# Performance work log

Hardware: AMD Instinct MI355X
Metric: run time of the kernel (lower is better)

Reference implementation:

```python
import jax, jax.numpy as jnp
import numpy as np

B, SQ, SK = 2, 2048, 2048
D, H = 1024, 16
HD = D // H              # head_dim = 64
R = 128                  # rel_pos_max_distance
P = 2 * R + 1            # num_pos_ids = 257
RADIUS = 256             # local_attention_radius


def setup_inputs() -> dict:
    key = jax.random.key(0)
    ks = jax.random.split(key, 8)
    s = 0.02
    return {
        "Q": jax.random.normal(ks[0], (B, SQ, D), dtype=jnp.float32),
        "K": jax.random.normal(ks[1], (B, SK, D), dtype=jnp.float32),
        "V": jax.random.normal(ks[2], (B, SK, D), dtype=jnp.float32),
        "Wq": jax.random.normal(ks[3], (D, D), dtype=jnp.float32) * s,
        "Wk": jax.random.normal(ks[4], (D, D), dtype=jnp.float32) * s,
        "Wv": jax.random.normal(ks[5], (D, D), dtype=jnp.float32) * s,
        "Wo": jax.random.normal(ks[6], (D, D), dtype=jnp.float32) * s,
        "E": jax.random.normal(ks[7], (P, D), dtype=jnp.float32) * s,  # rel_embeds
    }


def _split_heads(x, W):
    # bias-free projection then split: B x S x D -> B x H x S x HD
    y = x @ W.T
    b, s, _ = y.shape
    return y.reshape(b, s, H, HD).transpose(0, 2, 1, 3)


def reference(Q, K, V, Wq, Wk, Wv, Wo, E):
    q = _split_heads(Q, Wq)  # B,H,Sq,HD
    k = _split_heads(K, Wk)  # B,H,Sk,HD
    v = _split_heads(V, Wv)  # B,H,Sk,HD

    # rel_embeds reshape matches torch: E[p] viewed as (head_dim, num_heads)
    rel = E.reshape(P, HD, H).transpose(2, 0, 1)           # H,P,HD
    Q_rel = jnp.einsum("bhqd,hpd->bhqp", q, rel)           # B,H,Sq,P

    # slided relative position ids: clip(j - i, -R, R) + R
    i = jnp.arange(SQ)[:, None]
    j = jnp.arange(SK)[None, :]
    rel_ids = jnp.clip(j - i, -R, R) + R                   # Sq,Sk
    rel_shift = jnp.take_along_axis(
        Q_rel, jnp.broadcast_to(rel_ids, (B, H, SQ, SK)), axis=3
    )                                                       # B,H,Sq,Sk

    energy = (jnp.einsum("bhqd,bhkd->bhqk", q, k) + rel_shift) / jnp.sqrt(
        jnp.float32(HD)
    )

    # local attention mask: True = masked (outside window of radius RADIUS)
    mask = jnp.abs(j - i) > RADIUS                          # Sq,Sk
    mask = mask & ~jnp.all(mask, axis=-1, keepdims=True)    # never mask full rows
    energy = jnp.where(mask[None, None], -jnp.inf, energy)

    attn = jax.nn.softmax(energy, axis=-1)                  # B,H,Sq,Sk
    out = jnp.einsum("bhqk,bhkd->bhqd", attn, v)            # B,H,Sq,HD
    # torch: view(B,H,Sq,HD).permute(0,2,3,1).flatten(2,3) -> B,Sq,(HD*H)
    out = out.transpose(0, 2, 3, 1).reshape(B, SQ, D)
    return out @ Wo.T
```

## Files before the change

### kernel.cpp

```cpp
#include <hip/hip_runtime.h>
#include <hip/hip_bf16.h>

#define BATCH 2
#define SQn 2048
#define SKn 2048
#define DMODEL 1024
#define NH 16
#define HD 64
#define NPOS 257
#define RWIN 128
#define RADIUS 256

typedef __attribute__((ext_vector_type(8))) short bf16x8;
typedef __attribute__((ext_vector_type(4))) float f32x4;

static __device__ __forceinline__ unsigned short f2bf(float f) {
    union { float f; unsigned u; } v; v.f = f;
    unsigned r = (v.u + 0x7FFFu + ((v.u >> 16) & 1u)) >> 16;
    return (unsigned short)r;
}
static __device__ __forceinline__ float bf2f(unsigned short b) {
    union { unsigned u; float f; } v; v.u = ((unsigned)b) << 16;
    return v.f;
}

static __device__ __forceinline__ void gl_lds16(const unsigned short* g, unsigned short* l) {
    __builtin_amdgcn_global_load_lds(
        (const __attribute__((address_space(1))) unsigned*)g,
        (__attribute__((address_space(3))) unsigned*)l, 16, 0, 0);
}

#define SWZ(row) (((row) ^ ((row) >> 2)) & 3)

__global__ __launch_bounds__(256) void convert_kernel(
    const float* __restrict__ Q, const float* __restrict__ K, const float* __restrict__ V,
    const float* __restrict__ Wq, const float* __restrict__ Wk, const float* __restrict__ Wv,
    const float* __restrict__ Wo,
    unsigned short* __restrict__ xb,
    unsigned short* __restrict__ wb,
    unsigned short* __restrict__ wob)
{
    int i = blockIdx.x * 256 + threadIdx.x;
    const float* src;
    unsigned short* dst;
    int off;
    if (i < 3145728) {
        int which = i >> 20;
        off = i & 1048575;
        src = which == 0 ? Q : (which == 1 ? K : V);
        dst = xb + (size_t)which * 4194304;
    } else {
        int i2 = i - 3145728;
        int which = i2 >> 18;
        off = i2 & 262143;
        src = which == 0 ? Wq : (which == 1 ? Wk : (which == 2 ? Wv : Wo));
        dst = which < 3 ? wb + (size_t)which * 1048576 : wob;
    }
    float4 v4 = ((const float4*)src)[off];
    ushort4 o4;
    o4.x = f2bf(v4.x); o4.y = f2bf(v4.y); o4.z = f2bf(v4.z); o4.w = f2bf(v4.w);
    ((ushort4*)dst)[off] = o4;
}

__global__ __launch_bounds__(256) void mfma_gemm(
    const unsigned short* __restrict__ Xall,
    const unsigned short* __restrict__ Wall,
    unsigned short* __restrict__ Yall)
{
    __shared__ unsigned short sA[128 * 32];
    __shared__ unsigned short sB[128 * 32];
    __shared__ unsigned short sT[64 * 136];

    const int tid  = threadIdx.x;
    const int wv   = tid >> 6;
    const int lane = tid & 63;
    const int quad = lane >> 4;
    const int l15  = lane & 15;
    const int z    = blockIdx.z;
    const int m0   = blockIdx.x * 128;
    const int n0   = blockIdx.y * 128;
    const int wr   = (wv >> 1) * 64;
    const int wc   = (wv & 1) * 64;

    const unsigned short* X = Xall + (size_t)z * (4096 * 1024);
    const unsigned short* W = Wall + (size_t)z * (1024 * 1024);

    int aoff[4], boff[4];
#pragma unroll
    for (int t = 0; t < 4; ++t) {
        int row = wr + t * 16 + l15;
        aoff[t] = row * 32 + ((quad ^ SWZ(row)) * 8);
        int col = wc + t * 16 + l15;
        boff[t] = col * 32 + ((quad ^ SWZ(col)) * 8);
    }

    int srow[2], scg[2], sf[2];
#pragma unroll
    for (int r = 0; r < 2; ++r) {
        int f = r * 256 + tid;
        sf[r] = f;
        srow[r] = f >> 2;
        scg[r] = (f & 3) ^ SWZ(srow[r]);
    }

    f32x4 acc[4][4];
#pragma unroll
    for (int i = 0; i < 4; ++i)
#pragma unroll
        for (int j = 0; j < 4; ++j)
            acc[i][j] = (f32x4){0.f, 0.f, 0.f, 0.f};

    for (int k0 = 0; k0 < 1024; k0 += 32) {
        __syncthreads();
#pragma unroll
        for (int r = 0; r < 2; ++r) {
            gl_lds16(X + (size_t)(m0 + srow[r]) * 1024 + k0 + scg[r] * 8, &sA[sf[r] * 8]);
            gl_lds16(W + (size_t)(n0 + srow[r]) * 1024 + k0 + scg[r] * 8, &sB[sf[r] * 8]);
        }
        __syncthreads();

        bf16x8 af[4], bfr[4];
#pragma unroll
        for (int t = 0; t < 4; ++t) af[t]  = *(const bf16x8*)&sA[aoff[t]];
#pragma unroll
        for (int t = 0; t < 4; ++t) bfr[t] = *(const bf16x8*)&sB[boff[t]];
#pragma unroll
        for (int i = 0; i < 4; ++i)
#pragma unroll
            for (int j = 0; j < 4; ++j)
                acc[i][j] = __builtin_amdgcn_mfma_f32_16x16x32_bf16(af[i], bfr[j], acc[i][j], 0, 0, 0);
    }

    unsigned short* Y = Yall + (size_t)z * (4096 * 1024);
    const int b_ = m0 >> 11;
    const int s0 = m0 & (SQn - 1);

    if (z < 2) {
#pragma unroll
        for (int i = 0; i < 4; ++i) {
            int mbase = s0 + wr + i * 16 + quad * 4;
#pragma unroll
            for (int j = 0; j < 4; ++j) {
                int col = n0 + wc + j * 16 + l15;
                int h = col >> 6, dd = col & 63;
                unsigned short* yb = Y + (((size_t)(b_ * NH + h) * SQn) << 6) + dd;
#pragma unroll
                for (int r = 0; r < 4; ++r)
                    yb[(size_t)(mbase + r) << 6] = f2bf(acc[i][j][r]);
            }
        }
    } else {
#pragma unroll
        for (int hh = 0; hh < 2; ++hh) {
            __syncthreads();
            if ((wv & 1) == hh) {
#pragma unroll
                for (int i = 0; i < 4; ++i) {
                    int mloc = wr + i * 16 + quad * 4;
#pragma unroll
                    for (int j = 0; j < 4; ++j) {
                        ushort4 pk;
                        pk.x = f2bf(acc[i][j][0]);
                        pk.y = f2bf(acc[i][j][1]);
                        pk.z = f2bf(acc[i][j][2]);
                        pk.w = f2bf(acc[i][j][3]);
                        *(ushort4*)&sT[(j * 16 + l15) * 136 + mloc] = pk;
                    }
                }
            }
            __syncthreads();
            int h = (n0 >> 6) + hh;
            unsigned short* yb = Y + ((size_t)(b_ * NH + h) * HD) * SKn + s0;
#pragma unroll
            for (int it = 0; it < 4; ++it) {
                int u = it * 256 + tid;
                int dd = u >> 4, mc = u & 15;
                uint4 val = *(const uint4*)&sT[dd * 136 + mc * 8];
                *(uint4*)(yb + (size_t)dd * SKn + mc * 8) = val;
            }
        }
    }
}

__global__ __launch_bounds__(256) void gemm_out(
    const unsigned short* __restrict__ X,
    const unsigned short* __restrict__ W,
    float* __restrict__ Y)
{
    __shared__ unsigned short sA[64 * 32];
    __shared__ unsigned short sB[128 * 32];

    const int tid  = threadIdx.x;
    const int wv   = tid >> 6;
    const int lane = tid & 63;
    const int quad = lane >> 4;
    const int l15  = lane & 15;
    const int m0   = blockIdx.x * 64;
    const int n0   = blockIdx.y * 128;
    const int wr   = (wv >> 1) * 32;
    const int wc   = (wv & 1) * 64;

    int aoff[2], boff[4];
#pragma unroll
    for (int i = 0; i < 2; ++i) {
        int row = wr + i * 16 + l15;
        aoff[i] = row * 32 + ((quad ^ SWZ(row)) * 8);
    }
#pragma unroll
    for (int j = 0; j < 4; ++j) {
        int col = wc + j * 16 + l15;
        boff[j] = col * 32 + ((quad ^ SWZ(col)) * 8);
    }

    const int af_  = tid;
    const int arow = af_ >> 2;
    const int acs  = (af_ & 3) ^ SWZ(arow);
    int bf_[2], brow[2], bcs[2];
#pragma unroll
    for (int r = 0; r < 2; ++r) {
        int f = r * 256 + tid;
        bf_[r] = f; brow[r] = f >> 2; bcs[r] = (f & 3) ^ SWZ(brow[r]);
    }

    f32x4 acc[2][4];
#pragma unroll
    for (int i = 0; i < 2; ++i)
#pragma unroll
        for (int j = 0; j < 4; ++j)
            acc[i][j] = (f32x4){0.f, 0.f, 0.f, 0.f};

    for (int k0 = 0; k0 < 1024; k0 += 32) {
        __syncthreads();
        gl_lds16(X + (size_t)(m0 + arow) * 1024 + k0 + acs * 8, &sA[af_ * 8]);
#pragma unroll
        for (int r = 0; r < 2; ++r)
            gl_lds16(W + (size_t)(n0 + brow[r]) * 1024 + k0 + bcs[r] * 8, &sB[bf_[r] * 8]);
        __syncthreads();

        bf16x8 af[2], bfr[4];
#pragma unroll
        for (int i = 0; i < 2; ++i) af[i]  = *(const bf16x8*)&sA[aoff[i]];
#pragma unroll
        for (int j = 0; j < 4; ++j) bfr[j] = *(const bf16x8*)&sB[boff[j]];
#pragma unroll
        for (int i = 0; i < 2; ++i)
#pragma unroll
            for (int j = 0; j < 4; ++j)
                acc[i][j] = __builtin_amdgcn_mfma_f32_16x16x32_bf16(af[i], bfr[j], acc[i][j], 0, 0, 0);
    }

#pragma unroll
    for (int i = 0; i < 2; ++i) {
        int mbase = m0 + wr + i * 16 + quad * 4;
#pragma unroll
        for (int j = 0; j < 4; ++j) {
            int col = n0 + wc + j * 16 + l15;
#pragma unroll
            for (int r = 0; r < 4; ++r)
                Y[(size_t)(mbase + r) * DMODEL + col] = acc[i][j][r];
        }
    }
}

__global__ __launch_bounds__(256) void relt_kernel(
    const float* __restrict__ E, unsigned short* __restrict__ relTb)
{
    int idx = blockIdx.x * 256 + threadIdx.x;
    const int total = NH * NPOS * HD;
    if (idx < total) {
        int d = idx & (HD - 1);
        int p = (idx >> 6) % NPOS;
        int h = idx / (NPOS * HD);
        relTb[idx] = f2bf(E[(size_t)p * DMODEL + d * NH + h]);
    }
}

#define BIAS_S 9.765625e-4f

__global__ __launch_bounds__(256) void attn_mfma(
    const unsigned short* __restrict__ q,
    const unsigned short* __restrict__ k,
    const unsigned short* __restrict__ vT,
    const unsigned short* __restrict__ relTb,
    unsigned short* __restrict__ aob)
{
    __shared__ unsigned short sQ[64 * 64];
    __shared__ unsigned short sK[64 * 64];
    __shared__ unsigned short sVt[64 * 64];
    __shared__ unsigned short sP[4][16 * 72];
    __shared__ signed char    sq8[64 * 260];

    const int tid  = threadIdx.x;
    const int w    = tid >> 6;
    const int lane = tid & 63;
    const int quad = lane >> 4;
    const int l15  = lane & 15;
    const int xcd  = blockIdx.x & 7;
    const int sidx = blockIdx.x >> 3;
    const int bh   = (xcd << 2) | (sidx >> 5);
    const int q0   = (sidx & 31) << 6;
    const int h    = bh & (NH - 1);
    const int b    = bh >> 4;

    const int f1 = tid,       row1 = f1 >> 3;
    const int c1 = ((f1 & 7) ^ (row1 & 7)) * 8;
    const int f2 = 256 + tid, row2 = f2 >> 3;
    const int c2 = ((f2 & 7) ^ (row2 & 7)) * 8;

    {
        const unsigned short* gq = q + ((size_t)bh * SQn + q0) * HD;
        gl_lds16(gq + row1 * HD + c1, &sQ[f1 * 8]);
        gl_lds16(gq + row2 * HD + c2, &sQ[f2 * 8]);
    }
    __syncthreads();

    const int qrow = w * 16 + l15;
    const int qs = (quad ^ (qrow & 7)) * 8;
    bf16x8 a0 = *(const bf16x8*)&sQ[qrow * 64 + qs];
    bf16x8 a1 = *(const bf16x8*)&sQ[qrow * 64 + (qs ^ 32)];

    const int myrow = w * 16 + quad * 4;
    for (int c5 = 0; c5 < 5; ++c5) {
        __syncthreads();
        const unsigned short* gr = relTb + ((size_t)h * NPOS + c5 * 64) * HD;
        gl_lds16(gr + row1 * HD + c1, &sK[f1 * 8]);
        gl_lds16(gr + row2 * HD + c2, &sK[f2 * 8]);
        __syncthreads();
#pragma unroll
        for (int t = 0; t < 4; ++t) {
            int prow = t * 16 + l15;
            int ks = (quad ^ (prow & 7)) * 8;
            bf16x8 b0 = *(const bf16x8*)&sK[prow * 64 + ks];
            bf16x8 b1 = *(const bf16x8*)&sK[prow * 64 + (ks ^ 32)];
            f32x4 cc = {0.f, 0.f, 0.f, 0.f};
            cc = __builtin_amdgcn_mfma_f32_16x16x32_bf16(a0, b0, cc, 0, 0, 0);
            cc = __builtin_amdgcn_mfma_f32_16x16x32_bf16(a1, b1, cc, 0, 0, 0);
            int pos = c5 * 64 + t * 16 + l15;
            if (pos < NPOS) {
#pragma unroll
                for (int r = 0; r < 4; ++r) {
                    int iq = (int)rintf(cc[r] * 128.0f);
                    iq = iq < -127 ? -127 : (iq > 127 ? 127 : iq);
                    sq8[(myrow + r) * 260 + pos] = (signed char)iq;
                }
            }
        }
    }
    __syncthreads();

    float bias0[4], bias256[4];
#pragma unroll
    for (int r = 0; r < 4; ++r) {
        bias0[r]   = (float)sq8[(myrow + r) * 260 + 0]   * BIAS_S;
        bias256[r] = (float)sq8[(myrow + r) * 260 + 256] * BIAS_S;
    }

    const int lo = (q0 - RADIUS) > 0 ? (q0 - RADIUS) : 0;
    const int hi = (q0 + 63 + RADIUS) < (SKn - 1) ? (q0 + 63 + RADIUS) : (SKn - 1);
    const int nt = ((hi - lo) >> 6) + 1;
    const int e_ = l15 - quad * 4;

    const unsigned short* kg = k  + (size_t)bh * SKn * HD;
    const unsigned short* vg = vT + (size_t)bh * HD * SKn;

    float lacc[4] = {0.f, 0.f, 0.f, 0.f};
    f32x4 o[4];
#pragma unroll
    for (int t = 0; t < 4; ++t) o[t] = (f32x4){0.f, 0.f, 0.f, 0.f};

    {
        gl_lds16(kg + (size_t)(lo + row1) * HD + c1, &sK[f1 * 8]);
        gl_lds16(kg + (size_t)(lo + row2) * HD + c2, &sK[f2 * 8]);
        gl_lds16(vg + (size_t)row1 * SKn + lo + c1, &sVt[f1 * 8]);
        gl_lds16(vg + (size_t)row2 * SKn + lo + c2, &sVt[f2 * 8]);
    }

    for (int kt = 0; kt < nt; ++kt) {
        const int kb = lo + (kt << 6);
        __syncthreads();

        bf16x8 kf0[4], kf1[4], vf0[4], vf1[4];
#pragma unroll
        for (int t = 0; t < 4; ++t) {
            int prow = t * 16 + l15;
            int ks = (quad ^ (prow & 7)) * 8;
            kf0[t] = *(const bf16x8*)&sK[prow * 64 + ks];
            kf1[t] = *(const bf16x8*)&sK[prow * 64 + (ks ^ 32)];
            vf0[t] = *(const bf16x8*)&sVt[prow * 64 + ks];
            vf1[t] = *(const bf16x8*)&sVt[prow * 64 + (ks ^ 32)];
        }
        __syncthreads();

        if (kt + 1 < nt) {
            const int kb2 = kb + 64;
            gl_lds16(kg + (size_t)(kb2 + row1) * HD + c1, &sK[f1 * 8]);
            gl_lds16(kg + (size_t)(kb2 + row2) * HD + c2, &sK[f2 * 8]);
            gl_lds16(vg + (size_t)row1 * SKn + kb2 + c1, &sVt[f1 * 8]);
            gl_lds16(vg + (size_t)row2 * SKn + kb2 + c2, &sVt[f2 * 8]);
        }

        const int dtbase = kb - q0 - w * 16;
#pragma unroll
        for (int t = 0; t < 4; ++t) {
            const int dt = dtbase + t * 16;
            const int spb = (quad * 4) * 72 + t * 16 + l15;
            if (dt <= -272 || dt >= 272) {
#pragma unroll
                for (int r = 0; r < 4; ++r) sP[w][spb + r * 72] = 0;
            } else {
                f32x4 sc = {0.f, 0.f, 0.f, 0.f};
                sc = __builtin_amdgcn_mfma_f32_16x16x32_bf16(a0, kf0[t], sc, 0, 0, 0);
                sc = __builtin_amdgcn_mfma_f32_16x16x32_bf16(a1, kf1[t], sc, 0, 0, 0);

                float pv[4];
                if (dt >= -112 && dt <= 112) {
                    int idx0 = myrow * 260 + dt + 128 + e_;
#pragma unroll
                    for (int r = 0; r < 4; ++r) {
                        float bf = (float)sq8[idx0 + r * 259] * BIAS_S;
                        pv[r] = __expf(fmaf(sc[r], 0.125f, bf));
                    }
                } else if (dt >= -240 && dt <= -144) {
#pragma unroll
                    for (int r = 0; r < 4; ++r)
                        pv[r] = __expf(fmaf(sc[r], 0.125f, bias0[r]));
                } else if (dt >= 144 && dt <= 240) {
#pragma unroll
                    for (int r = 0; r < 4; ++r)
                        pv[r] = __expf(fmaf(sc[r], 0.125f, bias256[r]));
                } else {
#pragma unroll
                    for (int r = 0; r < 4; ++r) {
                        int d = dt + e_ - r;
                        bool in = (unsigned)(d + RADIUS) <= 2u * RADIUS;
                        int p = d < -RWIN ? 0 : (d > RWIN ? 2 * RWIN : d + RWIN);
                        float bf = (float)sq8[(myrow + r) * 260 + p] * BIAS_S;
                        float e = __expf(fmaf(sc[r], 0.125f, bf));
                        pv[r] = in ? e : 0.0f;
                    }
                }
#pragma unroll
                for (int r = 0; r < 4; ++r) {
                    unsigned short pb = f2bf(pv[r]);
                    sP[w][spb + r * 72] = pb;
                    lacc[r] += bf2f(pb);
                }
            }
        }

        bf16x8 p0 = *(const bf16x8*)&sP[w][l15 * 72 + quad * 8];
        bf16x8 p1 = *(const bf16x8*)&sP[w][l15 * 72 + 32 + quad * 8];
#pragma unroll
        for (int t = 0; t < 4; ++t) {
            o[t] = __builtin_amdgcn_mfma_f32_16x16x32_bf16(p0, vf0[t], o[t], 0, 0, 0);
            o[t] = __builtin_amdgcn_mfma_f32_16x16x32_bf16(p1, vf1[t], o[t], 0, 0, 0);
        }
    }

    float linv[4];
#pragma unroll
    for (int r = 0; r < 4; ++r) {
        float l = lacc[r];
#pragma unroll
        for (int off = 1; off <= 8; off <<= 1) l += __shfl_xor(l, off);
        linv[r] = 1.0f / l;
    }

#pragma unroll
    for (int t = 0; t < 4; ++t) {
#pragma unroll
        for (int r = 0; r < 4; ++r) {
            int i = q0 + w * 16 + quad * 4 + r;
            int c = (t * 16 + l15) * NH + h;
            aob[((size_t)b * SQn + i) * DMODEL + c] = f2bf(o[t][r] * linv[r]);
        }
    }
}

extern "C" void kernel_launch(void* const* d_in, const int* in_sizes, int n_in,
                              void* d_out, int out_size, void* d_ws, size_t ws_size,
                              hipStream_t stream) {
    const float* Q  = (const float*)d_in[0];
    const float* K  = (const float*)d_in[1];
    const float* V  = (const float*)d_in[2];
    const float* Wq = (const float*)d_in[3];
    const float* Wk = (const float*)d_in[4];
    const float* Wv = (const float*)d_in[5];
    const float* Wo = (const float*)d_in[6];
    const float* E  = (const float*)d_in[7];
    float* out = (float*)d_out;

    char* p = (char*)d_ws;
    unsigned short* xb    = (unsigned short*)p; p += (size_t)24 << 20;
    unsigned short* wb    = (unsigned short*)p; p += (size_t)6  << 20;
    unsigned short* wob   = (unsigned short*)p; p += (size_t)2  << 20;
    unsigned short* head  = (unsigned short*)p; p += (size_t)24 << 20;
    unsigned short* relTb = (unsigned short*)p; p += (size_t)1  << 20;
    unsigned short* aob   = (unsigned short*)p;

    unsigned short* qb  = head;
    unsigned short* kb  = head + 4194304;
    unsigned short* vTb = head + 8388608;

    dim3 bb(256);
    convert_kernel<<<dim3(16384), bb, 0, stream>>>(Q, K, V, Wq, Wk, Wv, Wo, xb, wb, wob);
    relt_kernel<<<dim3(1028), bb, 0, stream>>>(E, relTb);
    mfma_gemm<<<dim3(32, 8, 3), bb, 0, stream>>>(xb, wb, head);
    attn_mfma<<<dim3(BATCH * NH * (SQn / 64)), bb, 0, stream>>>(qb, kb, vTb, relTb, aob);
    gemm_out<<<dim3(64, 8), bb, 0, stream>>>(aob, wob, out);
}
```

Measured before the change: 226.5 us.

## Store attention output head-major and permute Wo to match in output GEMM

After: 212.4 us. 1.07x faster.

```diff
diff --git a/kernel.cpp b/kernel.cpp
--- a/kernel.cpp
+++ b/kernel.cpp
@@ -38,28 +38,42 @@
     const float* __restrict__ Wo,
     unsigned short* __restrict__ xb,
     unsigned short* __restrict__ wb,
-    unsigned short* __restrict__ wob)
+    unsigned short* __restrict__ woh)
 {
     int i = blockIdx.x * 256 + threadIdx.x;
-    const float* src;
-    unsigned short* dst;
-    int off;
     if (i < 3145728) {
         int which = i >> 20;
-        off = i & 1048575;
-        src = which == 0 ? Q : (which == 1 ? K : V);
-        dst = xb + (size_t)which * 4194304;
+        int off = i & 1048575;
+        const float* src = which == 0 ? Q : (which == 1 ? K : V);
+        unsigned short* dst = xb + (size_t)which * 4194304;
+        float4 v4 = ((const float4*)src)[off];
+        ushort4 o4;
+        o4.x = f2bf(v4.x); o4.y = f2bf(v4.y); o4.z = f2bf(v4.z); o4.w = f2bf(v4.w);
+        ((ushort4*)dst)[off] = o4;
     } else {
         int i2 = i - 3145728;
         int which = i2 >> 18;
-        off = i2 & 262143;
-        src = which == 0 ? Wq : (which == 1 ? Wk : (which == 2 ? Wv : Wo));
-        dst = which < 3 ? wb + (size_t)which * 1048576 : wob;
-    }
-    float4 v4 = ((const float4*)src)[off];
-    ushort4 o4;
-    o4.x = f2bf(v4.x); o4.y = f2bf(v4.y); o4.z = f2bf(v4.z); o4.w = f2bf(v4.w);
-    ((ushort4*)dst)[off] = o4;
+        int off = i2 & 262143;
+        if (which < 3) {
+            const float* src = which == 0 ? Wq : (which == 1 ? Wk : Wv);
+            unsigned short* dst = wb + (size_t)which * 1048576;
+            float4 v4 = ((const float4*)src)[off];
+            ushort4 o4;
+            o4.x = f2bf(v4.x); o4.y = f2bf(v4.y); o4.z = f2bf(v4.z); o4.w = f2bf(v4.w);
+            ((ushort4*)dst)[off] = o4;
+        } else {
+            float4 v4 = ((const float4*)Wo)[off];
+            int e0 = off * 4;
+            int n  = e0 >> 10;
+            int c0 = e0 & 1023;
+            int d  = c0 >> 4;
+            int h0 = c0 & 15;
+            woh[((size_t)(h0 + 0) * 1024 + n) * 64 + d] = f2bf(v4.x);
+            woh[((size_t)(h0 + 1) * 1024 + n) * 64 + d] = f2bf(v4.y);
+            woh[((size_t)(h0 + 2) * 1024 + n) * 64 + d] = f2bf(v4.z);
+            woh[((size_t)(h0 + 3) * 1024 + n) * 64 + d] = f2bf(v4.w);
+        }
+    }
 }
 
 __global__ __launch_bounds__(256) void mfma_gemm(
@@ -183,8 +197,8 @@
 }
 
 __global__ __launch_bounds__(256) void gemm_out(
-    const unsigned short* __restrict__ X,
-    const unsigned short* __restrict__ W,
+    const unsigned short* __restrict__ aoh,
+    const unsigned short* __restrict__ woh,
     float* __restrict__ Y)
 {
     __shared__ unsigned short sA[64 * 32];
@@ -199,6 +213,8 @@
     const int n0   = blockIdx.y * 128;
     const int wr   = (wv >> 1) * 32;
     const int wc   = (wv & 1) * 64;
+    const int b_   = m0 >> 11;
+    const int s0   = m0 & (SQn - 1);
 
     int aoff[2], boff[4];
 #pragma unroll
@@ -212,9 +228,8 @@
         boff[j] = col * 32 + ((quad ^ SWZ(col)) * 8);
     }
 
-    const int af_  = tid;
-    const int arow = af_ >> 2;
-    const int acs  = (af_ & 3) ^ SWZ(arow);
+    const int arow = tid >> 2;
+    const int acs  = (tid & 3) ^ SWZ(arow);
     int bf_[2], brow[2], bcs[2];
 #pragma unroll
     for (int r = 0; r < 2; ++r) {
@@ -229,24 +244,29 @@
         for (int j = 0; j < 4; ++j)
             acc[i][j] = (f32x4){0.f, 0.f, 0.f, 0.f};
 
-    for (int k0 = 0; k0 < 1024; k0 += 32) {
-        __syncthreads();
-        gl_lds16(X + (size_t)(m0 + arow) * 1024 + k0 + acs * 8, &sA[af_ * 8]);
-#pragma unroll
-        for (int r = 0; r < 2; ++r)
-            gl_lds16(W + (size_t)(n0 + brow[r]) * 1024 + k0 + bcs[r] * 8, &sB[bf_[r] * 8]);
-        __syncthreads();
-
-        bf16x8 af[2], bfr[4];
-#pragma unroll
-        for (int i = 0; i < 2; ++i) af[i]  = *(const bf16x8*)&sA[aoff[i]];
-#pragma unroll
-        for (int j = 0; j < 4; ++j) bfr[j] = *(const bf16x8*)&sB[boff[j]];
-#pragma unroll
-        for (int i = 0; i < 2; ++i)
-#pragma unroll
-            for (int j = 0; j < 4; ++j)
-                acc[i][j] = __builtin_amdgcn_mfma_f32_16x16x32_bf16(af[i], bfr[j], acc[i][j], 0, 0, 0);
+    for (int h = 0; h < NH; ++h) {
+        const unsigned short* Ah = aoh + ((size_t)(b_ * NH + h) * SQn + s0) * HD;
+        const unsigned short* Bh = woh + ((size_t)h * 1024 + n0) * HD;
+#pragma unroll
+        for (int k0 = 0; k0 < 64; k0 += 32) {
+            __syncthreads();
+            gl_lds16(Ah + (size_t)arow * HD + k0 + acs * 8, &sA[tid * 8]);
+#pragma unroll
+            for (int r = 0; r < 2; ++r)
+                gl_lds16(Bh + (size_t)brow[r] * HD + k0 + bcs[r] * 8, &sB[bf_[r] * 8]);
+            __syncthreads();
+
+            bf16x8 af[2], bfr[4];
+#pragma unroll
+            for (int i = 0; i < 2; ++i) af[i]  = *(const bf16x8*)&sA[aoff[i]];
+#pragma unroll
+            for (int j = 0; j < 4; ++j) bfr[j] = *(const bf16x8*)&sB[boff[j]];
+#pragma unroll
+            for (int i = 0; i < 2; ++i)
+#pragma unroll
+                for (int j = 0; j < 4; ++j)
+                    acc[i][j] = __builtin_amdgcn_mfma_f32_16x16x32_bf16(af[i], bfr[j], acc[i][j], 0, 0, 0);
+        }
     }
 
 #pragma unroll
@@ -282,7 +302,7 @@
     const unsigned short* __restrict__ k,
     const unsigned short* __restrict__ vT,
     const unsigned short* __restrict__ relTb,
-    unsigned short* __restrict__ aob)
+    unsigned short* __restrict__ aoh)
 {
     __shared__ unsigned short sQ[64 * 64];
     __shared__ unsigned short sK[64 * 64];
@@ -300,7 +320,6 @@
     const int bh   = (xcd << 2) | (sidx >> 5);
     const int q0   = (sidx & 31) << 6;
     const int h    = bh & (NH - 1);
-    const int b    = bh >> 4;
 
     const int f1 = tid,       row1 = f1 >> 3;
     const int c1 = ((f1 & 7) ^ (row1 & 7)) * 8;
@@ -466,13 +485,13 @@
         linv[r] = 1.0f / l;
     }
 
+    unsigned short* ob = aoh + ((size_t)bh * SQn + q0) * HD;
 #pragma unroll
     for (int t = 0; t < 4; ++t) {
 #pragma unroll
         for (int r = 0; r < 4; ++r) {
-            int i = q0 + w * 16 + quad * 4 + r;
-            int c = (t * 16 + l15) * NH + h;
-            aob[((size_t)b * SQn + i) * DMODEL + c] = f2bf(o[t][r] * linv[r]);
+            int irow = w * 16 + quad * 4 + r;
+            ob[irow * HD + t * 16 + l15] = f2bf(o[t][r] * linv[r]);
         }
     }
 }
@@ -493,19 +512,19 @@
     char* p = (char*)d_ws;
     unsigned short* xb    = (unsigned short*)p; p += (size_t)24 << 20;
     unsigned short* wb    = (unsigned short*)p; p += (size_t)6  << 20;
-    unsigned short* wob   = (unsigned short*)p; p += (size_t)2  << 20;
+    unsigned short* woh   = (unsigned short*)p; p += (size_t)2  << 20;
     unsigned short* head  = (unsigned short*)p; p += (size_t)24 << 20;
     unsigned short* relTb = (unsigned short*)p; p += (size_t)1  << 20;
-    unsigned short* aob   = (unsigned short*)p;
+    unsigned short* aoh   = (unsigned short*)p;
 
     unsigned short* qb  = head;
     unsigned short* kb  = head + 4194304;
     unsigned short* vTb = head + 8388608;
 
     dim3 bb(256);
-    convert_kernel<<<dim3(16384), bb, 0, stream>>>(Q, K, V, Wq, Wk, Wv, Wo, xb, wb, wob);
+    convert_kernel<<<dim3(16384), bb, 0, stream>>>(Q, K, V, Wq, Wk, Wv, Wo, xb, wb, woh);
     relt_kernel<<<dim3(1028), bb, 0, stream>>>(E, relTb);
     mfma_gemm<<<dim3(32, 8, 3), bb, 0, stream>>>(xb, wb, head);
-    attn_mfma<<<dim3(BATCH * NH * (SQn / 64)), bb, 0, stream>>>(qb, kb, vTb, relTb, aob);
-    gemm_out<<<dim3(64, 8), bb, 0, stream>>>(aob, wob, out);
-}
+    attn_mfma<<<dim3(BATCH * NH * (SQn / 64)), bb, 0, stream>>>(qb, kb, vTb, relTb, aoh);
+    gemm_out<<<dim3(64, 8), bb, 0, stream>>>(aoh, woh, out);
+}
```
